# Kernel optimization log

Hardware: AMD Instinct MI355X
Metric: run time of the kernel (lower is better)

Reference implementation:

```python
import jax, jax.numpy as jnp
import numpy as np

OVERLAP_THRESHOLD = 0.8
NUM_CLASSES = 1  # class-agnostic: class 0 = thing, class 1 = no-object


def setup_inputs() -> dict:
    key = jax.random.key(0)
    k1, k2 = jax.random.split(key)
    B, P, Q = 2, 200000, 100
    mask_cls = jax.random.normal(k1, (B, Q, NUM_CLASSES + 1), dtype=jnp.float32)
    mask_pred = jax.random.normal(k2, (B, P, Q), dtype=jnp.float32)
    pad = jnp.zeros((B, P), dtype=bool)  # no padded points -> static shapes
    return {"mask_cls": mask_cls, "mask_pred": mask_pred, "pad": pad}


def _panoptic_single(mask_cls, mask_pred):
    # mask_cls: [Q, C+1] logits, mask_pred: [P, Q] mask logits
    Q = mask_pred.shape[1]
    scores = mask_cls.max(-1)                     # [Q]
    labels = jnp.argmax(mask_cls, axis=-1)        # [Q]
    keep = labels != NUM_CLASSES                  # [Q] queries not predicted as no-object

    m = jax.nn.sigmoid(mask_pred)                 # [P, Q]
    # score-weighted masks; non-kept queries excluded via -inf (0 after softmax,
    # never selected by argmax) -- equivalent to torch's column subselection.
    prob = jnp.where(keep[None, :], scores[None, :] * m, -jnp.inf)  # [P, Q]
    probabilities = jax.nn.softmax(prob, axis=1)
    max_confs = probabilities.max(axis=1)         # [P]

    ids = jnp.argmax(prob, axis=1)                # [P] winning query per point
    ones = jnp.ones((mask_pred.shape[0],), dtype=jnp.int32)
    mask_area = jax.ops.segment_sum(ones, ids, num_segments=Q)      # (cur_mask_ids == k).sum()

    orig_bin = m >= 0.5                           # [P, Q]
    orig_area = orig_bin.astype(jnp.int32).sum(axis=0)              # (cur_masks[:, k] >= 0.5).sum()
    point_bin = jnp.take_along_axis(orig_bin, ids[:, None], axis=1)[:, 0]  # [P]
    mask_count = jax.ops.segment_sum(point_bin.astype(jnp.int32), ids, num_segments=Q)

    ratio = mask_area.astype(jnp.float32) / jnp.maximum(orig_area, 1).astype(jnp.float32)
    accepted = (keep & (mask_area > 0) & (orig_area > 0) & (mask_count > 0)
                & (ratio >= OVERLAP_THRESHOLD))   # [Q]

    # sequential segment_id assignment == cumulative count of accepted queries
    # (all queries are 'things'; masks are disjoint since they come from argmax)
    seg_id = jnp.where(accepted, jnp.cumsum(accepted.astype(jnp.int32)), 0)  # [Q]

    point_valid = accepted[ids] & point_bin       # [P] (cur_mask_ids==k) & (mask>=0.5) & accepted
    ins = jnp.where(point_valid, seg_id[ids], 0).astype(jnp.int32)
    sem = jnp.where(point_valid, labels[ids], 0).astype(jnp.int32)
    return sem, ins, max_confs


def reference(mask_cls, mask_pred, pad):
    # pad is all-False (no padded points), so mask_pred[~pad] is identity and
    # shapes stay static; pad is accepted for signature fidelity.
    del pad
    sem, ins, max_confs = jax.vmap(_panoptic_single)(mask_cls, mask_pred)
    return sem, ins, max_confs
```

## Files before the change

### kernel.cpp

```cpp
#include <hip/hip_runtime.h>
#include <cstdint>
#include <cstddef>

#define BB 2
#define PP 200000
#define QQ 100
#define TPB 256
#define NBX ((PP + TPB - 1) / TPB)


__global__ __launch_bounds__(TPB, 3) void stats_kernel(
    const float* __restrict__ mask_cls,
    const float* __restrict__ mask_pred,
    float* __restrict__ out_conf,
    int* __restrict__ ws_ids,
    int* __restrict__ g_cnt)
{
    __shared__ float s_score[QQ];
    __shared__ int s_cnt[3 * QQ];

    const int b = blockIdx.y;
    const int t = threadIdx.x;

    if (t < QQ) {
        float c0 = mask_cls[(b * QQ + t) * 2 + 0];
        float c1 = mask_cls[(b * QQ + t) * 2 + 1];
        bool keep = !(c1 > c0);
        s_score[t] = keep ? fmaxf(c0, c1) : -INFINITY;
    }
    for (int i = t; i < 3 * QQ; i += TPB) s_cnt[i] = 0;
    __syncthreads();

    const int p = blockIdx.x * TPB + t;
    const bool valid = p < PP;
    const int pc = valid ? p : (PP - 1);
    const float4* __restrict__ row =
        reinterpret_cast<const float4*>(mask_pred + ((size_t)b * PP + pc) * QQ);

    float4 r[QQ / 4];
#pragma unroll
    for (int i = 0; i < QQ / 4; ++i) r[i] = row[i];

    float best = -INFINITY;
    int bestq = -1, bestbin = 0;
    float sumexp = 0.f;

#pragma unroll
    for (int i = 0; i < QQ / 4; ++i) {
        const float4 x4 = r[i];
        const float xs[4] = {x4.x, x4.y, x4.z, x4.w};
#pragma unroll
        for (int c = 0; c < 4; ++c) {
            const int q = i * 4 + c;
            const float sc = s_score[q];
            if (sc == -INFINITY) continue;

            const float x = xs[c];
            float sig = 1.0f / (1.0f + expf(-x));
            const int bin = (sig >= 0.5f) ? 1 : 0;

            unsigned long long mb = __ballot(bin && valid);
            if ((t & 63) == 0 && mb)
                atomicAdd(&s_cnt[q], __popcll(mb));

            sig = fmaxf(sig, 1e-38f);
            const float v = sc * sig;
            sumexp += __expf(v);
            if (v > best) { best = v; bestq = q; bestbin = bin; }
        }
    }
    if (bestq < 0) {
        bestq = 0;
        float sig0 = 1.0f / (1.0f + expf(-r[0].x));
        bestbin = (sig0 >= 0.5f) ? 1 : 0;
    }

    if (valid) {
        atomicAdd(&s_cnt[QQ + bestq], 1);
        if (bestbin) atomicAdd(&s_cnt[2 * QQ + bestq], 1);
        out_conf[(size_t)b * PP + p] = __expf(best) / sumexp;
        ws_ids[(size_t)b * PP + p] = (bestq << 1) | bestbin;
    }
    __syncthreads();

    for (int i = t; i < 3 * QQ; i += TPB)
        if (s_cnt[i]) atomicAdd(&g_cnt[b * 3 * QQ + i], s_cnt[i]);
}

__global__ __launch_bounds__(256) void finalize_kernel(
    const float* __restrict__ mask_cls,
    const int* __restrict__ g_cnt,
    int* __restrict__ ws_tab)
{
    __shared__ int s_acc[BB][QQ];
    __shared__ int s_lab[BB][QQ];
    const int t = threadIdx.x;

    if (t < BB * QQ) {
        const int b = t / QQ, q = t % QQ;
        float c0 = mask_cls[(b * QQ + q) * 2 + 0];
        float c1 = mask_cls[(b * QQ + q) * 2 + 1];
        bool keep = !(c1 > c0);
        int oa = g_cnt[b * 3 * QQ + q];
        int ma = g_cnt[b * 3 * QQ + QQ + q];
        int mc = g_cnt[b * 3 * QQ + 2 * QQ + q];
        float ratio = (float)ma / (float)max(oa, 1);
        bool acc = keep && (ma > 0) && (oa > 0) && (mc > 0) && (ratio >= 0.8f);
        s_acc[b][q] = acc ? 1 : 0;
        s_lab[b][q] = (c1 > c0) ? 1 : 0;
    }
    __syncthreads();

    if (t < BB) {
        int run = 0;
        for (int q = 0; q < QQ; ++q) {
            int a = s_acc[t][q];
            run += a;
            ws_tab[t * QQ + q]           = a ? s_lab[t][q] : 0;
            ws_tab[BB * QQ + t * QQ + q] = a ? run : 0;
        }
    }
}

__global__ __launch_bounds__(TPB) void scatter_kernel(
    const int* __restrict__ ws_ids,
    const int* __restrict__ ws_tab,
    float* __restrict__ out_sem,
    float* __restrict__ out_ins)
{
    __shared__ float s_sem[QQ], s_ins[QQ];
    const int b = blockIdx.y;
    const int t = threadIdx.x;
    if (t < QQ) {
        s_sem[t] = (float)ws_tab[b * QQ + t];
        s_ins[t] = (float)ws_tab[BB * QQ + b * QQ + t];
    }
    __syncthreads();

    const int p = blockIdx.x * TPB + t;
    if (p < PP) {
        const int v = ws_ids[(size_t)b * PP + p];
        const int bin = v & 1;
        const int q = v >> 1;
        out_sem[(size_t)b * PP + p] = bin ? s_sem[q] : 0.0f;
        out_ins[(size_t)b * PP + p] = bin ? s_ins[q] : 0.0f;
    }
}

extern "C" void kernel_launch(void* const* d_in, const int* in_sizes, int n_in,
                              void* d_out, int out_size, void* d_ws, size_t ws_size,
                              hipStream_t stream) {
    const float* mask_cls  = (const float*)d_in[0];
    const float* mask_pred = (const float*)d_in[1];

    float* out = (float*)d_out;
    int* ws = (int*)d_ws;
    int* g_cnt  = ws;
    int* ws_tab = g_cnt + BB * 3 * QQ;
    int* ws_ids = ws_tab + 2 * BB * QQ;

    hipMemsetAsync(g_cnt, 0, BB * 3 * QQ * sizeof(int), stream);

    dim3 grid(NBX, BB);
    stats_kernel<<<grid, TPB, 0, stream>>>(
        mask_cls, mask_pred, out + 2 * (size_t)BB * PP, ws_ids, g_cnt);
    finalize_kernel<<<1, 256, 0, stream>>>(mask_cls, g_cnt, ws_tab);
    scatter_kernel<<<grid, TPB, 0, stream>>>(
        ws_ids, ws_tab, out, out + (size_t)BB * PP);
}
```

Measured before the change: 257.6 us.

## Fold finalize into scatter and replace per-query shared atomics with lane-owned counters

The stats kernel now keeps each query's orig_area popcount in a register owned by one lane, with two counters covering queries 0-63 and 64-99. It issues only two shared atomics per lane at the end instead of one per query per wave. Scores are read from shared memory as float4, the skip for non-kept queries is removed, and the minimum-occupancy hint is dropped from launch_bounds. The finalize kernel is folded into the scatter kernel: every block recomputes the acceptance table and prefix sum on one thread, which saves a launch but adds a serial 100-step loop per block.

Measured after the change: 309.3 us. 1.2x slower.

```diff
diff --git a/kernel.cpp b/kernel.cpp
--- a/kernel.cpp
+++ b/kernel.cpp
@@ -9,24 +9,26 @@
 #define NBX ((PP + TPB - 1) / TPB)
 
 
-__global__ __launch_bounds__(TPB, 3) void stats_kernel(
+__global__ __launch_bounds__(TPB) void stats_kernel(
     const float* __restrict__ mask_cls,
     const float* __restrict__ mask_pred,
     float* __restrict__ out_conf,
     int* __restrict__ ws_ids,
     int* __restrict__ g_cnt)
 {
-    __shared__ float s_score[QQ];
+    __shared__ float4 s_score4[QQ / 4];
     __shared__ int s_cnt[3 * QQ];
 
     const int b = blockIdx.y;
     const int t = threadIdx.x;
+    const int lane = t & 63;
 
+    float* s_scoref = reinterpret_cast<float*>(s_score4);
     if (t < QQ) {
         float c0 = mask_cls[(b * QQ + t) * 2 + 0];
         float c1 = mask_cls[(b * QQ + t) * 2 + 1];
         bool keep = !(c1 > c0);
-        s_score[t] = keep ? fmaxf(c0, c1) : -INFINITY;
+        s_scoref[t] = keep ? fmaxf(c0, c1) : -INFINITY;
     }
     for (int i = t; i < 3 * QQ; i += TPB) s_cnt[i] = 0;
     __syncthreads();
@@ -42,29 +44,30 @@
     for (int i = 0; i < QQ / 4; ++i) r[i] = row[i];
 
     float best = -INFINITY;
+    float sumexp = 0.f;
     int bestq = -1, bestbin = 0;
-    float sumexp = 0.f;
+    int corig0 = 0, corig1 = 0;
 
 #pragma unroll
     for (int i = 0; i < QQ / 4; ++i) {
         const float4 x4 = r[i];
-        const float xs[4] = {x4.x, x4.y, x4.z, x4.w};
+        const float4 sc4 = s_score4[i];
+        const float xs[4]  = {x4.x, x4.y, x4.z, x4.w};
+        const float scs[4] = {sc4.x, sc4.y, sc4.z, sc4.w};
 #pragma unroll
         for (int c = 0; c < 4; ++c) {
             const int q = i * 4 + c;
-            const float sc = s_score[q];
-            if (sc == -INFINITY) continue;
-
             const float x = xs[c];
             float sig = 1.0f / (1.0f + expf(-x));
             const int bin = (sig >= 0.5f) ? 1 : 0;
 
             unsigned long long mb = __ballot(bin && valid);
-            if ((t & 63) == 0 && mb)
-                atomicAdd(&s_cnt[q], __popcll(mb));
+            const int pcnt = __popcll(mb);
+            if (q < 64) corig0 += (lane == q)      ? pcnt : 0;
+            else        corig1 += (lane == q - 64) ? pcnt : 0;
 
-            sig = fmaxf(sig, 1e-38f);
-            const float v = sc * sig;
+            float sg = fmaxf(sig, 1e-38f);
+            const float v = scs[c] * sg;
             sumexp += __expf(v);
             if (v > best) { best = v; bestq = q; bestbin = bin; }
         }
@@ -74,6 +77,9 @@
         float sig0 = 1.0f / (1.0f + expf(-r[0].x));
         bestbin = (sig0 >= 0.5f) ? 1 : 0;
     }
+
+    atomicAdd(&s_cnt[lane], corig0);
+    if (lane < QQ - 64) atomicAdd(&s_cnt[64 + lane], corig1);
 
     if (valid) {
         atomicAdd(&s_cnt[QQ + bestq], 1);
@@ -87,53 +93,39 @@
         if (s_cnt[i]) atomicAdd(&g_cnt[b * 3 * QQ + i], s_cnt[i]);
 }
 
-__global__ __launch_bounds__(256) void finalize_kernel(
+__global__ __launch_bounds__(TPB) void scatter_kernel(
     const float* __restrict__ mask_cls,
     const int* __restrict__ g_cnt,
-    int* __restrict__ ws_tab)
-{
-    __shared__ int s_acc[BB][QQ];
-    __shared__ int s_lab[BB][QQ];
-    const int t = threadIdx.x;
-
-    if (t < BB * QQ) {
-        const int b = t / QQ, q = t % QQ;
-        float c0 = mask_cls[(b * QQ + q) * 2 + 0];
-        float c1 = mask_cls[(b * QQ + q) * 2 + 1];
-        bool keep = !(c1 > c0);
-        int oa = g_cnt[b * 3 * QQ + q];
-        int ma = g_cnt[b * 3 * QQ + QQ + q];
-        int mc = g_cnt[b * 3 * QQ + 2 * QQ + q];
-        float ratio = (float)ma / (float)max(oa, 1);
-        bool acc = keep && (ma > 0) && (oa > 0) && (mc > 0) && (ratio >= 0.8f);
-        s_acc[b][q] = acc ? 1 : 0;
-        s_lab[b][q] = (c1 > c0) ? 1 : 0;
-    }
-    __syncthreads();
-
-    if (t < BB) {
-        int run = 0;
-        for (int q = 0; q < QQ; ++q) {
-            int a = s_acc[t][q];
-            run += a;
-            ws_tab[t * QQ + q]           = a ? s_lab[t][q] : 0;
-            ws_tab[BB * QQ + t * QQ + q] = a ? run : 0;
-        }
-    }
-}
-
-__global__ __launch_bounds__(TPB) void scatter_kernel(
     const int* __restrict__ ws_ids,
-    const int* __restrict__ ws_tab,
     float* __restrict__ out_sem,
     float* __restrict__ out_ins)
 {
+    __shared__ int s_acc[QQ], s_lab[QQ];
     __shared__ float s_sem[QQ], s_ins[QQ];
     const int b = blockIdx.y;
     const int t = threadIdx.x;
+
     if (t < QQ) {
-        s_sem[t] = (float)ws_tab[b * QQ + t];
-        s_ins[t] = (float)ws_tab[BB * QQ + b * QQ + t];
+        float c0 = mask_cls[(b * QQ + t) * 2 + 0];
+        float c1 = mask_cls[(b * QQ + t) * 2 + 1];
+        bool keep = !(c1 > c0);
+        int oa = g_cnt[b * 3 * QQ + t];
+        int ma = g_cnt[b * 3 * QQ + QQ + t];
+        int mc = g_cnt[b * 3 * QQ + 2 * QQ + t];
+        float ratio = (float)ma / (float)max(oa, 1);
+        bool acc = keep && (ma > 0) && (oa > 0) && (mc > 0) && (ratio >= 0.8f);
+        s_acc[t] = acc ? 1 : 0;
+        s_lab[t] = (c1 > c0) ? 1 : 0;
+    }
+    __syncthreads();
+    if (t == 0) {
+        int run = 0;
+        for (int q = 0; q < QQ; ++q) {
+            int a = s_acc[q];
+            run += a;
+            s_sem[q] = a ? (float)s_lab[q] : 0.0f;
+            s_ins[q] = a ? (float)run : 0.0f;
+        }
     }
     __syncthreads();
 
@@ -156,15 +148,13 @@
     float* out = (float*)d_out;
     int* ws = (int*)d_ws;
     int* g_cnt  = ws;
-    int* ws_tab = g_cnt + BB * 3 * QQ;
-    int* ws_ids = ws_tab + 2 * BB * QQ;
+    int* ws_ids = g_cnt + BB * 3 * QQ;
 
     hipMemsetAsync(g_cnt, 0, BB * 3 * QQ * sizeof(int), stream);
 
     dim3 grid(NBX, BB);
     stats_kernel<<<grid, TPB, 0, stream>>>(
         mask_cls, mask_pred, out + 2 * (size_t)BB * PP, ws_ids, g_cnt);
-    finalize_kernel<<<1, 256, 0, stream>>>(mask_cls, g_cnt, ws_tab);
     scatter_kernel<<<grid, TPB, 0, stream>>>(
-        ws_ids, ws_tab, out, out + (size_t)BB * PP);
+        mask_cls, g_cnt, ws_ids, out, out + (size_t)BB * PP);
 }
```
